# Performance work log

Hardware: AMD Instinct MI355X
Metric: run time of the kernel (lower is better)

The kernel has to match this reference:

```python
import jax, jax.numpy as jnp
import numpy as np

N_NODES = 50000
N_EDGES = 800000
X_DIM = 128         # node feature dim
HID = 128           # hidden_channels == edge_attr channels
IN_CH = X_DIM + HID # MLP in_channels = 256
OUT_CH = 128


def setup_inputs() -> dict:
    key = jax.random.key(0)
    ks = jax.random.split(key, 10)
    x = jax.random.normal(ks[0], (N_NODES, X_DIM), dtype=jnp.float32)
    edge_index = jax.random.randint(ks[1], (2, N_EDGES), 0, N_NODES, dtype=jnp.int64)
    edge_attr = jax.random.normal(ks[2], (N_EDGES, HID), dtype=jnp.float32)
    # MLP params (stored as [in, out]); scale like torch Linear default init
    def lin(k, fan_in, fan_out):
        k1, k2 = jax.random.split(k)
        bound = 1.0 / np.sqrt(fan_in)
        W = jax.random.uniform(k1, (fan_in, fan_out), minval=-bound, maxval=bound, dtype=jnp.float32)
        b = jax.random.uniform(k2, (fan_out,), minval=-bound, maxval=bound, dtype=jnp.float32)
        return W, b
    W0, b0 = lin(ks[3], IN_CH, HID)
    W2, b2 = lin(ks[4], HID, HID)
    W3, b3 = lin(ks[5], HID, OUT_CH)
    return {"x": x, "edge_index": edge_index, "edge_attr": edge_attr,
            "W0": W0, "b0": b0, "W2": W2, "b2": b2, "W3": W3, "b3": b3}


def reference(x, edge_index, edge_attr, W0, b0, W2, b2, W3, b3):
    # edge_sum[n, c] = sum over edges e with edge_index[0, e] == n of edge_attr[e, c]
    # (equivalent to the per-channel sparse COO @ ones loop, fused across channels)
    edge_sum = jax.ops.segment_sum(edge_attr, edge_index[0], num_segments=x.shape[0])
    inputs = jnp.concatenate([x, edge_sum], axis=1)  # [N, in_channels]
    h = jax.nn.elu(inputs @ W0 + b0)
    h = jax.nn.elu(h @ W2 + b2)
    out = h @ W3 + b3
    return out
```

## Files before the change

kernel.cpp:

```cpp
#include <hip/hip_runtime.h>
#include <cmath>

typedef __attribute__((ext_vector_type(8))) short bf16x8;
typedef __attribute__((ext_vector_type(4))) float f32x4;

__device__ __forceinline__ short f2bf(float f) {
    unsigned u = __builtin_bit_cast(unsigned, f);
    u += 0x7fff + ((u >> 16) & 1);
    return (short)(u >> 16);
}

__global__ __launch_bounds__(256)
void hist_kernel(const int* __restrict__ dst, int* __restrict__ counts, int E)
{
    int e = blockIdx.x * 256 + threadIdx.x;
    if (e < E) atomicAdd(&counts[dst[e]], 1);
}

#define SCAN_B 256

__global__ __launch_bounds__(SCAN_B)
void scan_p1_kernel(const int* __restrict__ counts, int* __restrict__ offsets,
                    int* __restrict__ blockSums, int N)
{
    __shared__ int sh[SCAN_B];
    const int t = threadIdx.x;
    const int i = blockIdx.x * SCAN_B + t;
    int v = (i < N) ? counts[i] : 0;
    sh[t] = v;
    __syncthreads();
    for (int d = 1; d < SCAN_B; d <<= 1) {
        int u = (t >= d) ? sh[t - d] : 0;
        __syncthreads();
        sh[t] += u;
        __syncthreads();
    }
    if (i < N) offsets[i] = sh[t] - v;
    if (t == SCAN_B - 1) blockSums[blockIdx.x] = sh[SCAN_B - 1];
}

__global__ __launch_bounds__(SCAN_B)
void scan_p2_kernel(int* __restrict__ blockSums, int nblk)
{
    __shared__ int sh[SCAN_B];
    const int t = threadIdx.x;
    int v = (t < nblk) ? blockSums[t] : 0;
    sh[t] = v;
    __syncthreads();
    for (int d = 1; d < SCAN_B; d <<= 1) {
        int u = (t >= d) ? sh[t - d] : 0;
        __syncthreads();
        sh[t] += u;
        __syncthreads();
    }
    if (t < nblk) blockSums[t] = sh[t] - v;
}

__global__ __launch_bounds__(SCAN_B)
void scan_p3_kernel(int* __restrict__ offsets, const int* __restrict__ blockSums,
                    int* __restrict__ cursor, int N, int E)
{
    const int i = blockIdx.x * SCAN_B + threadIdx.x;
    if (i < N) {
        int o = offsets[i] + blockSums[blockIdx.x];
        offsets[i] = o;
        cursor[i]  = o;
    }
    if (i == 0) offsets[N] = E;
}

__global__ __launch_bounds__(256)
void scatter_perm_kernel(const int* __restrict__ dst, int* __restrict__ cursor,
                         int* __restrict__ perm, int E)
{
    int e = blockIdx.x * 256 + threadIdx.x;
    if (e < E) {
        int p = atomicAdd(&cursor[dst[e]], 1);
        perm[p] = e;
    }
}

__global__ __launch_bounds__(256)
void gather_sum_kernel(const float* __restrict__ edge_attr,
                       const int* __restrict__ perm,
                       const int* __restrict__ offsets,
                       float* __restrict__ edge_sum, int N)
{
    const int wid  = (blockIdx.x * 256 + threadIdx.x) >> 6;
    const int lane = threadIdx.x & 63;
    if (wid >= N) return;
    const int beg = offsets[wid];
    const int end = offsets[wid + 1];
    const int half = lane >> 5;
    const int li   = lane & 31;

    float4 acc = make_float4(0.f, 0.f, 0.f, 0.f);
    for (int base = beg; base < end; base += 64) {
        const int m = (end - base < 64) ? (end - base) : 64;
        int eid = 0;
        if (lane < m) eid = perm[base + lane];
        const int pairs = (m + 1) >> 1;
        #pragma unroll 4
        for (int j = 0; j < pairs; ++j) {
            const int idx = 2 * j + half;
            const int e = __shfl(eid, idx, 64);
            if (idx < m) {
                const float4 v = *reinterpret_cast<const float4*>(
                    &edge_attr[(size_t)e * 128 + li * 4]);
                acc.x += v.x; acc.y += v.y; acc.z += v.z; acc.w += v.w;
            }
        }
    }
    float4 other;
    other.x = __shfl(acc.x, li + 32, 64);
    other.y = __shfl(acc.y, li + 32, 64);
    other.z = __shfl(acc.z, li + 32, 64);
    other.w = __shfl(acc.w, li + 32, 64);
    if (half == 0) {
        acc.x += other.x; acc.y += other.y; acc.z += other.z; acc.w += other.w;
        *reinterpret_cast<float4*>(&edge_sum[(size_t)wid * 128 + li * 4]) = acc;
    }
}

__device__ __forceinline__ void stage_W(const float* __restrict__ W, int krow0,
                                        short* __restrict__ Wt, int tid)
{
    #pragma unroll
    for (int i = 0; i < 16; ++i) {
        int p = tid + i * 512;
        int n = p & 127;
        int k = (p >> 7) << 1;
        float a = W[(size_t)(krow0 + k) * 128 + n];
        float b = W[(size_t)(krow0 + k + 1) * 128 + n];
        int grp = (k >> 3) ^ (n & 15);
        ushort2 s;
        s.x = (unsigned short)f2bf(a);
        s.y = (unsigned short)f2bf(b);
        *reinterpret_cast<ushort2*>(&Wt[n * 128 + grp * 8 + (k & 7)]) = s;
    }
}

__global__ __launch_bounds__(512, 2)
void fused_mlp_kernel(const float* __restrict__ x,
                      const float* __restrict__ edge_sum,
                      const float* __restrict__ W0, const float* __restrict__ b0,
                      const float* __restrict__ W2, const float* __restrict__ b2,
                      const float* __restrict__ W3, const float* __restrict__ b3,
                      float* __restrict__ out, int N)
{
    __shared__ short At[128 * 128];
    __shared__ short Wt[128 * 128];

    const int tid  = threadIdx.x;
    const int lane = tid & 63;
    const int wv   = tid >> 6;
    const int l15  = lane & 15;
    const int quad = lane >> 4;
    const int m0   = wv * 16;
    const int blockRow = blockIdx.x * 128;

    f32x4 acc[8];
    #pragma unroll
    for (int nt = 0; nt < 8; ++nt) acc[nt] = (f32x4){0.f, 0.f, 0.f, 0.f};

    for (int half = 0; half < 2; ++half) {
        const float* Asrc = half ? edge_sum : x;
        __syncthreads();
        #pragma unroll
        for (int i = 0; i < 8; ++i) {
            int f  = tid + i * 512;
            int r  = f >> 5;
            int c4 = (f & 31) << 2;
            int g  = blockRow + r; if (g >= N) g = N - 1;
            const float4 v = *reinterpret_cast<const float4*>(&Asrc[(size_t)g * 128 + c4]);
            int grp = (c4 >> 3) ^ (r & 15);
            ushort4 s;
            s.x = (unsigned short)f2bf(v.x);
            s.y = (unsigned short)f2bf(v.y);
            s.z = (unsigned short)f2bf(v.z);
            s.w = (unsigned short)f2bf(v.w);
            *reinterpret_cast<ushort4*>(&At[r * 128 + grp * 8 + (c4 & 7)]) = s;
        }
        stage_W(W0, half * 128, Wt, tid);
        __syncthreads();
        #pragma unroll
        for (int ks = 0; ks < 4; ++ks) {
            int g = ks * 4 + quad;
            int so = ((g ^ l15) << 3);
            bf16x8 a = *reinterpret_cast<bf16x8*>(&At[(m0 + l15) * 128 + so]);
            #pragma unroll
            for (int nt = 0; nt < 8; ++nt) {
                bf16x8 b = *reinterpret_cast<bf16x8*>(&Wt[(nt * 16 + l15) * 128 + so]);
                acc[nt] = __builtin_amdgcn_mfma_f32_16x16x32_bf16(a, b, acc[nt], 0, 0, 0);
            }
        }
    }

    __syncthreads();
    #pragma unroll
    for (int nt = 0; nt < 8; ++nt) {
        float bv = b0[nt * 16 + l15];
        #pragma unroll
        for (int r = 0; r < 4; ++r) {
            float v = acc[nt][r] + bv;
            v = (v > 0.f) ? v : (__expf(v) - 1.f);
            int m = m0 + quad * 4 + r;
            int c = nt * 16 + l15;
            int grp = (c >> 3) ^ (m & 15);
            At[m * 128 + grp * 8 + (c & 7)] = f2bf(v);
        }
        acc[nt] = (f32x4){0.f, 0.f, 0.f, 0.f};
    }
    stage_W(W2, 0, Wt, tid);
    __syncthreads();

    #pragma unroll
    for (int ks = 0; ks < 4; ++ks) {
        int g = ks * 4 + quad;
        int so = ((g ^ l15) << 3);
        bf16x8 a = *reinterpret_cast<bf16x8*>(&At[(m0 + l15) * 128 + so]);
        #pragma unroll
        for (int nt = 0; nt < 8; ++nt) {
            bf16x8 b = *reinterpret_cast<bf16x8*>(&Wt[(nt * 16 + l15) * 128 + so]);
            acc[nt] = __builtin_amdgcn_mfma_f32_16x16x32_bf16(a, b, acc[nt], 0, 0, 0);
        }
    }

    __syncthreads();
    #pragma unroll
    for (int nt = 0; nt < 8; ++nt) {
        float bv = b2[nt * 16 + l15];
        #pragma unroll
        for (int r = 0; r < 4; ++r) {
            float v = acc[nt][r] + bv;
            v = (v > 0.f) ? v : (__expf(v) - 1.f);
            int m = m0 + quad * 4 + r;
            int c = nt * 16 + l15;
            int grp = (c >> 3) ^ (m & 15);
            At[m * 128 + grp * 8 + (c & 7)] = f2bf(v);
        }
        acc[nt] = (f32x4){0.f, 0.f, 0.f, 0.f};
    }
    stage_W(W3, 0, Wt, tid);
    __syncthreads();

    #pragma unroll
    for (int ks = 0; ks < 4; ++ks) {
        int g = ks * 4 + quad;
        int so = ((g ^ l15) << 3);
        bf16x8 a = *reinterpret_cast<bf16x8*>(&At[(m0 + l15) * 128 + so]);
        #pragma unroll
        for (int nt = 0; nt < 8; ++nt) {
            bf16x8 b = *reinterpret_cast<bf16x8*>(&Wt[(nt * 16 + l15) * 128 + so]);
            acc[nt] = __builtin_amdgcn_mfma_f32_16x16x32_bf16(a, b, acc[nt], 0, 0, 0);
        }
    }

    #pragma unroll
    for (int nt = 0; nt < 8; ++nt) {
        float bv = b3[nt * 16 + l15];
        #pragma unroll
        for (int r = 0; r < 4; ++r) {
            int gr = blockRow + m0 + quad * 4 + r;
            if (gr < N) out[(size_t)gr * 128 + nt * 16 + l15] = acc[nt][r] + bv;
        }
    }
}

extern "C" void kernel_launch(void* const* d_in, const int* in_sizes, int n_in,
                              void* d_out, int out_size, void* d_ws, size_t ws_size,
                              hipStream_t stream)
{
    const float* x     = (const float*)d_in[0];
    const int*   eidx  = (const int*)d_in[1];
    const float* eattr = (const float*)d_in[2];
    const float* W0 = (const float*)d_in[3];
    const float* b0 = (const float*)d_in[4];
    const float* W2 = (const float*)d_in[5];
    const float* b2 = (const float*)d_in[6];
    const float* W3 = (const float*)d_in[7];
    const float* b3 = (const float*)d_in[8];
    float* out = (float*)d_out;

    const int N = in_sizes[0] / 128;
    const int E = in_sizes[2] / 128;

    int* counts    = (int*)d_ws;
    int* offsets   = counts + N;
    int* cursor    = offsets + (N + 1);
    int* blockSums = cursor + N;
    int* perm      = blockSums + 256;
    uintptr_t p = (uintptr_t)(perm + E);
    p = (p + 255) & ~(uintptr_t)255;
    float* edge_sum = (float*)p;

    hipMemsetAsync(counts, 0, (size_t)N * sizeof(int), stream);

    const int eblocks = (E + 255) / 256;
    const int nblk    = (N + SCAN_B - 1) / SCAN_B;

    hist_kernel<<<eblocks, 256, 0, stream>>>(eidx, counts, E);
    scan_p1_kernel<<<nblk, SCAN_B, 0, stream>>>(counts, offsets, blockSums, N);
    scan_p2_kernel<<<1, SCAN_B, 0, stream>>>(blockSums, nblk);
    scan_p3_kernel<<<nblk, SCAN_B, 0, stream>>>(offsets, blockSums, cursor, N, E);
    scatter_perm_kernel<<<eblocks, 256, 0, stream>>>(eidx, cursor, perm, E);
    {
        int gthreads = N * 64;
        int gblocks = (gthreads + 255) / 256;
        gather_sum_kernel<<<gblocks, 256, 0, stream>>>(eattr, perm, offsets, edge_sum, N);
    }

    int mblocks = (N + 127) / 128;
    fused_mlp_kernel<<<mblocks, 512, 0, stream>>>(x, edge_sum, W0, b0, W2, b2,
                                                  W3, b3, out, N);
}
```

Measured before the change: 723.0 us.

## Fuse edge-attribute gather-sum into MLP kernel, removing edge_sum buffer

```diff
diff --git a/kernel.cpp b/kernel.cpp
--- a/kernel.cpp
+++ b/kernel.cpp
@@ -77,48 +77,6 @@
     if (e < E) {
         int p = atomicAdd(&cursor[dst[e]], 1);
         perm[p] = e;
-    }
-}
-
-__global__ __launch_bounds__(256)
-void gather_sum_kernel(const float* __restrict__ edge_attr,
-                       const int* __restrict__ perm,
-                       const int* __restrict__ offsets,
-                       float* __restrict__ edge_sum, int N)
-{
-    const int wid  = (blockIdx.x * 256 + threadIdx.x) >> 6;
-    const int lane = threadIdx.x & 63;
-    if (wid >= N) return;
-    const int beg = offsets[wid];
-    const int end = offsets[wid + 1];
-    const int half = lane >> 5;
-    const int li   = lane & 31;
-
-    float4 acc = make_float4(0.f, 0.f, 0.f, 0.f);
-    for (int base = beg; base < end; base += 64) {
-        const int m = (end - base < 64) ? (end - base) : 64;
-        int eid = 0;
-        if (lane < m) eid = perm[base + lane];
-        const int pairs = (m + 1) >> 1;
-        #pragma unroll 4
-        for (int j = 0; j < pairs; ++j) {
-            const int idx = 2 * j + half;
-            const int e = __shfl(eid, idx, 64);
-            if (idx < m) {
-                const float4 v = *reinterpret_cast<const float4*>(
-                    &edge_attr[(size_t)e * 128 + li * 4]);
-                acc.x += v.x; acc.y += v.y; acc.z += v.z; acc.w += v.w;
-            }
-        }
-    }
-    float4 other;
-    other.x = __shfl(acc.x, li + 32, 64);
-    other.y = __shfl(acc.y, li + 32, 64);
-    other.z = __shfl(acc.z, li + 32, 64);
-    other.w = __shfl(acc.w, li + 32, 64);
-    if (half == 0) {
-        acc.x += other.x; acc.y += other.y; acc.z += other.z; acc.w += other.w;
-        *reinterpret_cast<float4*>(&edge_sum[(size_t)wid * 128 + li * 4]) = acc;
     }
 }
 
@@ -142,7 +100,9 @@
 
 __global__ __launch_bounds__(512, 2)
 void fused_mlp_kernel(const float* __restrict__ x,
-                      const float* __restrict__ edge_sum,
+                      const float* __restrict__ edge_attr,
+                      const int* __restrict__ perm,
+                      const int* __restrict__ offsets,
                       const float* __restrict__ W0, const float* __restrict__ b0,
                       const float* __restrict__ W2, const float* __restrict__ b2,
                       const float* __restrict__ W3, const float* __restrict__ b3,
@@ -158,41 +118,94 @@
     const int quad = lane >> 4;
     const int m0   = wv * 16;
     const int blockRow = blockIdx.x * 128;
+    const int half32 = lane >> 5;
+    const int li     = lane & 31;
 
     f32x4 acc[8];
     #pragma unroll
     for (int nt = 0; nt < 8; ++nt) acc[nt] = (f32x4){0.f, 0.f, 0.f, 0.f};
 
-    for (int half = 0; half < 2; ++half) {
-        const float* Asrc = half ? edge_sum : x;
-        __syncthreads();
-        #pragma unroll
-        for (int i = 0; i < 8; ++i) {
-            int f  = tid + i * 512;
-            int r  = f >> 5;
-            int c4 = (f & 31) << 2;
-            int g  = blockRow + r; if (g >= N) g = N - 1;
-            const float4 v = *reinterpret_cast<const float4*>(&Asrc[(size_t)g * 128 + c4]);
-            int grp = (c4 >> 3) ^ (r & 15);
+    #pragma unroll
+    for (int i = 0; i < 8; ++i) {
+        int f  = tid + i * 512;
+        int r  = f >> 5;
+        int c4 = (f & 31) << 2;
+        int g  = blockRow + r; if (g >= N) g = N - 1;
+        const float4 v = *reinterpret_cast<const float4*>(&x[(size_t)g * 128 + c4]);
+        int grp = (c4 >> 3) ^ (r & 15);
+        ushort4 s;
+        s.x = (unsigned short)f2bf(v.x);
+        s.y = (unsigned short)f2bf(v.y);
+        s.z = (unsigned short)f2bf(v.z);
+        s.w = (unsigned short)f2bf(v.w);
+        *reinterpret_cast<ushort4*>(&At[r * 128 + grp * 8 + (c4 & 7)]) = s;
+    }
+    stage_W(W0, 0, Wt, tid);
+    __syncthreads();
+    #pragma unroll
+    for (int ks = 0; ks < 4; ++ks) {
+        int g = ks * 4 + quad;
+        int so = ((g ^ l15) << 3);
+        bf16x8 a = *reinterpret_cast<bf16x8*>(&At[(m0 + l15) * 128 + so]);
+        #pragma unroll
+        for (int nt = 0; nt < 8; ++nt) {
+            bf16x8 b = *reinterpret_cast<bf16x8*>(&Wt[(nt * 16 + l15) * 128 + so]);
+            acc[nt] = __builtin_amdgcn_mfma_f32_16x16x32_bf16(a, b, acc[nt], 0, 0, 0);
+        }
+    }
+    __syncthreads();
+
+    stage_W(W0, 128, Wt, tid);
+    for (int r = 0; r < 16; ++r) {
+        const int g = blockRow + m0 + r;
+        float4 a4 = make_float4(0.f, 0.f, 0.f, 0.f);
+        if (g < N) {
+            const int beg = offsets[g];
+            const int end = offsets[g + 1];
+            for (int base = beg; base < end; base += 64) {
+                const int m = (end - base < 64) ? (end - base) : 64;
+                int eid = 0;
+                if (lane < m) eid = perm[base + lane];
+                const int pairs = (m + 1) >> 1;
+                #pragma unroll 4
+                for (int j = 0; j < pairs; ++j) {
+                    const int idx = 2 * j + half32;
+                    const int e = __shfl(eid, idx, 64);
+                    if (idx < m) {
+                        const float4 v = *reinterpret_cast<const float4*>(
+                            &edge_attr[(size_t)e * 128 + li * 4]);
+                        a4.x += v.x; a4.y += v.y; a4.z += v.z; a4.w += v.w;
+                    }
+                }
+            }
+        }
+        float4 o;
+        o.x = __shfl(a4.x, li + 32, 64);
+        o.y = __shfl(a4.y, li + 32, 64);
+        o.z = __shfl(a4.z, li + 32, 64);
+        o.w = __shfl(a4.w, li + 32, 64);
+        if (half32 == 0) {
+            a4.x += o.x; a4.y += o.y; a4.z += o.z; a4.w += o.w;
+            const int rg  = m0 + r;
+            const int grp = (li >> 1) ^ (rg & 15);
             ushort4 s;
-            s.x = (unsigned short)f2bf(v.x);
-            s.y = (unsigned short)f2bf(v.y);
-            s.z = (unsigned short)f2bf(v.z);
-            s.w = (unsigned short)f2bf(v.w);
-            *reinterpret_cast<ushort4*>(&At[r * 128 + grp * 8 + (c4 & 7)]) = s;
-        }
-        stage_W(W0, half * 128, Wt, tid);
-        __syncthreads();
-        #pragma unroll
-        for (int ks = 0; ks < 4; ++ks) {
-            int g = ks * 4 + quad;
-            int so = ((g ^ l15) << 3);
-            bf16x8 a = *reinterpret_cast<bf16x8*>(&At[(m0 + l15) * 128 + so]);
-            #pragma unroll
-            for (int nt = 0; nt < 8; ++nt) {
-                bf16x8 b = *reinterpret_cast<bf16x8*>(&Wt[(nt * 16 + l15) * 128 + so]);
-                acc[nt] = __builtin_amdgcn_mfma_f32_16x16x32_bf16(a, b, acc[nt], 0, 0, 0);
-            }
+            s.x = (unsigned short)f2bf(a4.x);
+            s.y = (unsigned short)f2bf(a4.y);
+            s.z = (unsigned short)f2bf(a4.z);
+            s.w = (unsigned short)f2bf(a4.w);
+            *reinterpret_cast<ushort4*>(&At[rg * 128 + grp * 8 + (li & 1) * 4]) = s;
+        }
+    }
+    __syncthreads();
+    #pragma unroll
+    for (int ks = 0; ks < 4; ++ks) {
+        int g = ks * 4 + quad;
+        int so = ((g ^ l15) << 3);
+        bf16x8 a = *reinterpret_cast<bf16x8*>(&At[(m0 + l15) * 128 + so]);
+        #pragma unroll
+        for (int nt = 0; nt < 8; ++nt) {
+            bf16x8 b = *reinterpret_cast<bf16x8*>(&Wt[(nt * 16 + l15) * 128 + so]);
+            acc[nt] = __builtin_amdgcn_mfma_f32_16x16x32_bf16(a, b, acc[nt], 0, 0, 0);
         }
     }
 
@@ -290,9 +303,6 @@
     int* cursor    = offsets + (N + 1);
     int* blockSums = cursor + N;
     int* perm      = blockSums + 256;
-    uintptr_t p = (uintptr_t)(perm + E);
-    p = (p + 255) & ~(uintptr_t)255;
-    float* edge_sum = (float*)p;
 
     hipMemsetAsync(counts, 0, (size_t)N * sizeof(int), stream);
 
@@ -304,13 +314,8 @@
     scan_p2_kernel<<<1, SCAN_B, 0, stream>>>(blockSums, nblk);
     scan_p3_kernel<<<nblk, SCAN_B, 0, stream>>>(offsets, blockSums, cursor, N, E);
     scatter_perm_kernel<<<eblocks, 256, 0, stream>>>(eidx, cursor, perm, E);
-    {
-        int gthreads = N * 64;
-        int gblocks = (gthreads + 255) / 256;
-        gather_sum_kernel<<<gblocks, 256, 0, stream>>>(eattr, perm, offsets, edge_sum, N);
-    }
 
     int mblocks = (N + 127) / 128;
-    fused_mlp_kernel<<<mblocks, 512, 0, stream>>>(x, edge_sum, W0, b0, W2, b2,
-                                                  W3, b3, out, N);
-}
+    fused_mlp_kernel<<<mblocks, 512, 0, stream>>>(x, eattr, perm, offsets,
+                                                  W0, b0, W2, b2, W3, b3, out, N);
+}
```

After: 785.7 us. 1.09x slower.
